# Kernel optimization log

Measured on AMD Instinct MI355X. Metric: run time of the kernel, lower is better.

Reference implementation:

```python
import jax, jax.numpy as jnp
import numpy as np

B, S, D = 8, 2048, 1024  # batch, seq_len, emb_dim == qkv_dim
NEG = -999999.0  # module uses -999999 instead of -inf


def setup_inputs() -> dict:
    key = jax.random.key(0)
    ks = jax.random.split(key, 4)
    inputs = jax.random.normal(ks[0], (B, S, D), dtype=jnp.float32)
    # causal mask, flax attention layout [B, 1, S, S]
    causal = jnp.tril(jnp.ones((S, S), dtype=bool))
    mask = jnp.broadcast_to(causal, (B, 1, S, S))
    scale = 1.0 / np.sqrt(D)
    Wq = jax.random.normal(ks[1], (D, D), dtype=jnp.float32) * scale
    Wk = jax.random.normal(ks[2], (D, D), dtype=jnp.float32) * scale
    Wv = jax.random.normal(ks[3], (D, D), dtype=jnp.float32) * scale
    z = jnp.zeros((D,), dtype=jnp.float32)
    return {"inputs": inputs, "mask": mask, "Wq": Wq, "bq": z, "Wk": Wk,
            "bk": z, "Wv": Wv, "bv": z}


def reference(inputs, mask, Wq, bq, Wk, bk, Wv, bv):
    q = inputs @ Wq + bq  # [B,S,D]
    k = inputs @ Wk + bk
    v = inputs @ Wv + bv
    depth = q.shape[-1]
    q = q / jnp.sqrt(jnp.asarray(depth, q.dtype))
    attn = jnp.einsum('bqd,bkd->bqk', q, k)  # [B,S,S]
    attn = jnp.where(jnp.squeeze(mask, axis=1), attn, NEG)
    attn = jax.nn.softmax(attn, axis=-1)
    return attn @ v  # [B,S,D]
```

## Files before the change

kernel.cpp:

```cpp
#include <hip/hip_runtime.h>
#include <hip/hip_bf16.h>
#include <cstdint>

#define S_LEN 2048
#define D_DIM 1024
#define NB 8

typedef __attribute__((ext_vector_type(8))) short bf16x8;
typedef __attribute__((ext_vector_type(4))) float f32x4;

__device__ __forceinline__ unsigned short f2bf(float f) {
  union { float f; unsigned u; } x; x.f = f;
  unsigned r = x.u + 0x7fffu + ((x.u >> 16) & 1u);
  return (unsigned short)(r >> 16);
}
__device__ __forceinline__ float bf2f(unsigned short b) {
  union { unsigned u; float f; } x; x.u = ((unsigned)b) << 16;
  return x.f;
}
__device__ __forceinline__ void gload16(const void* g, void* l) {
  __builtin_amdgcn_global_load_lds((const __attribute__((address_space(1))) void*)g,
                                   (__attribute__((address_space(3))) void*)l, 16, 0, 0);
}

__global__ __launch_bounds__(256)
void cvt_f32_bf16(const float* __restrict__ in, unsigned short* __restrict__ out, int n4) {
  int i = blockIdx.x * blockDim.x + threadIdx.x;
  if (i >= n4) return;
  float4 v = reinterpret_cast<const float4*>(in)[i];
  ushort4 o;
  o.x = f2bf(v.x); o.y = f2bf(v.y); o.z = f2bf(v.z); o.w = f2bf(v.w);
  reinterpret_cast<ushort4*>(out)[i] = o;
}

__global__ __launch_bounds__(256)
void transpose_f32_bf16(const float* __restrict__ in, unsigned short* __restrict__ out,
                        int rows, int cols) {
  __shared__ unsigned short tile[32][33];
  int bx = blockIdx.x * 32, by = blockIdx.y * 32;
  int tx = threadIdx.x, ty = threadIdx.y;
  #pragma unroll
  for (int i = ty; i < 32; i += 8)
    tile[i][tx] = f2bf(in[(size_t)(by + i) * cols + bx + tx]);
  __syncthreads();
  #pragma unroll
  for (int i = ty; i < 32; i += 8)
    out[(size_t)(bx + i) * rows + by + tx] = tile[tx][i];
}

__global__ __launch_bounds__(256)
void transpose_bf16(const unsigned short* __restrict__ in, unsigned short* __restrict__ out,
                    int ldin, int ldout, long zin, long zout) {
  __shared__ unsigned short tile[32][33];
  const unsigned short* ip = in + (size_t)blockIdx.z * zin;
  unsigned short* op = out + (size_t)blockIdx.z * zout;
  int bx = blockIdx.x * 32, by = blockIdx.y * 32;
  int tx = threadIdx.x, ty = threadIdx.y;
  #pragma unroll
  for (int i = ty; i < 32; i += 8)
    tile[i][tx] = ip[(size_t)(by + i) * ldin + bx + tx];
  __syncthreads();
  #pragma unroll
  for (int i = ty; i < 32; i += 8)
    op[(size_t)(bx + i) * ldout + by + tx] = tile[tx][i];
}

__global__ __launch_bounds__(256)
void combine_pv(float* __restrict__ O, const unsigned short* __restrict__ part,
                const float* __restrict__ rs) {
  int i = blockIdx.x * 256 + threadIdx.x;
  if (i >= 2097152) return;
  int e = i * 4;
  int z = e >> 20;
  int rem = e & 1048575;
  int r = rem >> 10;
  int col = rem & 1023;
  float inv = 1.f / rs[z * S_LEN + 1024 + r];
  float4 o = *reinterpret_cast<const float4*>(&O[(size_t)z * S_LEN * D_DIM + (size_t)(1024 + r) * 1024 + col]);
  ushort4 p = *reinterpret_cast<const ushort4*>(&part[((size_t)z * 1024 + r) * 1024 + col]);
  o.x = (o.x + bf2f(p.x)) * inv;
  o.y = (o.y + bf2f(p.y)) * inv;
  o.z = (o.z + bf2f(p.z)) * inv;
  o.w = (o.w + bf2f(p.w)) * inv;
  *reinterpret_cast<float4*>(&O[(size_t)z * S_LEN * D_DIM + (size_t)(1024 + r) * 1024 + col]) = o;
}

template<int MODE>
__global__ __launch_bounds__(512, 2)
void gemm8(const unsigned short* __restrict__ Aall, const unsigned short* __restrict__ Btall,
           void* __restrict__ Call, int Kd, int lda, int ldb, int ldc,
           long sAz, long sBz, long sCz,
           const float* __restrict__ b0, const float* __restrict__ b1,
           const float* __restrict__ b2, float* __restrict__ rowsum,
           unsigned short* __restrict__ part, int ntn) {
  __shared__ __align__(16) unsigned short As[4][8192];
  __shared__ __align__(16) unsigned short Bs[4][8192];
  int nwg = gridDim.x, bid = blockIdx.x;
  int wg = (bid & 7) * (nwg >> 3) + (bid >> 3);
  int z, tm, tn, kt0, nkt, m2c = 0;
  if (MODE == 0) {
    z = 0; tm = wg / ntn; tn = wg % ntn; kt0 = 0; nkt = Kd >> 5;
  } else if (MODE == 1) {
    z = wg / 36; int f = wg % 36;
    tm = 0;
    while ((tm + 1) * (tm + 2) / 2 <= f) ++tm;
    tn = f - tm * (tm + 1) / 2;
    kt0 = 0; nkt = Kd >> 5;
  } else {
    z = wg / 48; int r = wg % 48; tn = r / 12; int f = r % 12;
    const int tmT[12] = {0,1,2,3,4,4,5,5,6,6,7,7};
    const int cT[12]  = {0,0,0,0,0,1,0,1,0,1,0,1};
    tm = tmT[f]; int c = cT[f];
    int kts = (tm + 1) * 8;
    if (tm < 4) { kt0 = 0; nkt = kts; m2c = 0; }
    else { int half = kts >> 1; kt0 = c ? half : 0; nkt = c ? (kts - half) : half; m2c = 1 + c; }
  }
  const unsigned short* A  = Aall  + (size_t)z * sAz;
  const unsigned short* Bt = Btall + (size_t)z * sBz;
  int m0 = tm * 256, n0 = tn * 256;
  int t = threadIdx.x, lane = t & 63, w = t >> 6;
  int wr = w >> 2, wc = w & 3;
  int lr = lane & 15, lq = lane >> 4;
  long triBase = (long)(tm * (tm + 1) / 2) * 65536;

  int offA[8], offB[4];
  #pragma unroll
  for (int mi = 0; mi < 8; ++mi) {
    int row = wr * 128 + mi * 16 + lr;
    offA[mi] = row * 32 + ((lq ^ ((row >> 1) & 3)) * 8);
  }
  #pragma unroll
  for (int ni = 0; ni < 4; ++ni) {
    int row = wc * 64 + ni * 16 + lr;
    offB[ni] = row * 32 + ((lq ^ ((row >> 1) & 3)) * 8);
  }
  int srow[2], soff[2];
  #pragma unroll
  for (int c = 0; c < 2; ++c) {
    int r = c * 128 + w * 16 + (lane >> 2);
    srow[c] = r;
    soff[c] = ((lane & 3) ^ ((r >> 1) & 3)) * 8;
  }

  f32x4 acc[8][4];
  f32x4 zero4 = {0.f, 0.f, 0.f, 0.f};
  #pragma unroll
  for (int mi = 0; mi < 8; ++mi)
    #pragma unroll
    for (int ni = 0; ni < 4; ++ni) acc[mi][ni] = zero4;

  auto stgA = [&](int buf, int kg) {
    #pragma unroll
    for (int c = 0; c < 2; ++c) {
      const unsigned short* src;
      if (MODE == 2)
        src = A + triBase + (long)(kg >> 3) * 65536 + srow[c] * 256 + (kg & 7) * 32 + soff[c];
      else
        src = A + (size_t)(m0 + srow[c]) * lda + kg * 32 + soff[c];
      gload16(src, &As[buf][c * 4096 + w * 512]);
    }
  };
  auto stgB = [&](int buf, int kg) {
    #pragma unroll
    for (int c = 0; c < 2; ++c)
      gload16(Bt + (size_t)(n0 + srow[c]) * ldb + kg * 32 + soff[c],
              &Bs[buf][c * 4096 + w * 512]);
  };

  stgA(0, kt0); stgB(0, kt0); stgA(1, kt0 + 1); stgB(1, kt0 + 1);
  asm volatile("s_waitcnt vmcnt(4)" ::: "memory");
  __builtin_amdgcn_s_barrier();

  for (int i = 0; i < nkt; ++i) {
    const int bcur = i & 3, bpre = (i + 2) & 3;
    const bool stg = (i + 2 < nkt);
    const int kg = kt0 + i;
    const unsigned short* Ac = As[bcur];
    const unsigned short* Bc = Bs[bcur];
    bf16x8 af[4], bfv[4];

    #pragma unroll
    for (int q = 0; q < 4; ++q) af[q]  = *reinterpret_cast<const bf16x8*>(&Ac[offA[q]]);
    #pragma unroll
    for (int q = 0; q < 4; ++q) bfv[q] = *reinterpret_cast<const bf16x8*>(&Bc[offB[q]]);
    if (stg) stgA(bpre, kg + 2);
    __builtin_amdgcn_s_barrier();
    asm volatile("s_waitcnt lgkmcnt(0)" ::: "memory");
    __builtin_amdgcn_sched_barrier(0);
    __builtin_amdgcn_s_setprio(1);
    #pragma unroll
    for (int q = 0; q < 4; ++q)
      #pragma unroll
      for (int j = 0; j < 4; ++j)
        acc[q][j] = __builtin_amdgcn_mfma_f32_16x16x32_bf16(af[q], bfv[j], acc[q][j], 0, 0, 0);
    __builtin_amdgcn_s_setprio(0);
    __builtin_amdgcn_s_barrier();

    #pragma unroll
    for (int q = 0; q < 4; ++q) af[q] = *reinterpret_cast<const bf16x8*>(&Ac[offA[4 + q]]);
    if (stg) stgB(bpre, kg + 2);
    if (i + 2 < nkt)      asm volatile("s_waitcnt vmcnt(4)" ::: "memory");
    else if (i + 1 < nkt) asm volatile("s_waitcnt vmcnt(0)" ::: "memory");
    __builtin_amdgcn_s_barrier();
    asm volatile("s_waitcnt lgkmcnt(0)" ::: "memory");
    __builtin_amdgcn_sched_barrier(0);
    __builtin_amdgcn_s_setprio(1);
    #pragma unroll
    for (int q = 0; q < 4; ++q)
      #pragma unroll
      for (int j = 0; j < 4; ++j)
        acc[4 + q][j] = __builtin_amdgcn_mfma_f32_16x16x32_bf16(af[q], bfv[j], acc[4 + q][j], 0, 0, 0);
    __builtin_amdgcn_s_setprio(0);
    __builtin_amdgcn_s_barrier();
  }
  __syncthreads();

  unsigned short* ep = &As[0][0] + w * 4096;
  int lq4 = lq << 4;

  if (MODE == 0) {
    unsigned short* C = (unsigned short*)Call;
    #pragma unroll
    for (int mh = 0; mh < 2; ++mh) {
      #pragma unroll
      for (int mi2 = 0; mi2 < 4; ++mi2)
        #pragma unroll
        for (int ni = 0; ni < 4; ++ni) {
          int col = ni * 16 + lr;
          int gcol = n0 + wc * 64 + col;
          float bb, sc;
          if (gcol < 1024)      { bb = b0[gcol];        sc = 0.03125f; }
          else if (gcol < 2048) { bb = b1[gcol - 1024]; sc = 1.0f; }
          else                  { bb = b2[gcol - 2048]; sc = 1.0f; }
          #pragma unroll
          for (int j = 0; j < 4; ++j) {
            int lrow = mi2 * 16 + lq * 4 + j;
            ep[lrow * 64 + (col ^ lq4)] = f2bf((acc[mh * 4 + mi2][ni][j] + bb) * sc);
          }
        }
      asm volatile("s_waitcnt lgkmcnt(0)" ::: "memory");
      #pragma unroll
      for (int pass = 0; pass < 8; ++pass) {
        int rrow = pass * 8 + (lane >> 3);
        int c8 = (lane & 7) * 8;
        int sw = ((rrow >> 2) & 3) << 4;
        bf16x8 vv = *reinterpret_cast<const bf16x8*>(&ep[rrow * 64 + (c8 ^ sw)]);
        int grow = m0 + wr * 128 + mh * 64 + rrow;
        *reinterpret_cast<bf16x8*>(&C[(size_t)grow * ldc + n0 + wc * 64 + c8]) = vv;
      }
      asm volatile("s_waitcnt lgkmcnt(0)" ::: "memory");
    }
  } else if (MODE == 1) {
    unsigned short* Ct = (unsigned short*)Call + (size_t)z * sCz + triBase + (long)tn * 65536;
    float* rs = rowsum + z * S_LEN;
    #pragma unroll
    for (int mh = 0; mh < 2; ++mh) {
      #pragma unroll
      for (int mi2 = 0; mi2 < 4; ++mi2)
        #pragma unroll
        for (int j = 0; j < 4; ++j) {
          int lrow = mi2 * 16 + lq * 4 + j;
          int grow = m0 + wr * 128 + mh * 64 + lrow;
          float partial = 0.f;
          #pragma unroll
          for (int ni = 0; ni < 4; ++ni) {
            int col = ni * 16 + lr;
            int gcol = n0 + wc * 64 + col;
            float e = (gcol <= grow) ? __expf(acc[mh * 4 + mi2][ni][j]) : 0.f;
            partial += e;
            ep[lrow * 64 + (col ^ lq4)] = f2bf(e);
          }
          #pragma unroll
          for (int off = 1; off < 16; off <<= 1) partial += __shfl_xor(partial, off);
          if (lr == 0) atomicAdd(&rs[grow], partial);
        }
      asm volatile("s_waitcnt lgkmcnt(0)" ::: "memory");
      #pragma unroll
      for (int pass = 0; pass < 8; ++pass) {
        int rrow = pass * 8 + (lane >> 3);
        int c8 = (lane & 7) * 8;
        int sw = ((rrow >> 2) & 3) << 4;
        bf16x8 vv = *reinterpret_cast<const bf16x8*>(&ep[rrow * 64 + (c8 ^ sw)]);
        int lrow2 = wr * 128 + mh * 64 + rrow;
        *reinterpret_cast<bf16x8*>(&Ct[(size_t)lrow2 * 256 + wc * 64 + c8]) = vv;
      }
      asm volatile("s_waitcnt lgkmcnt(0)" ::: "memory");
    }
  } else {
    float* C = (float*)Call + (size_t)z * sCz;
    const float* rs = rowsum + z * S_LEN;
    #pragma unroll
    for (int mi = 0; mi < 8; ++mi)
      #pragma unroll
      for (int j = 0; j < 4; ++j) {
        int row = m0 + wr * 128 + mi * 16 + lq * 4 + j;
        if (m2c == 0) {
          float inv = 1.f / rs[row];
          #pragma unroll
          for (int ni = 0; ni < 4; ++ni) {
            int col = n0 + wc * 64 + ni * 16 + lr;
            C[(size_t)row * ldc + col] = acc[mi][ni][j] * inv;
          }
        } else if (m2c == 1) {
          #pragma unroll
          for (int ni = 0; ni < 4; ++ni) {
            int col = n0 + wc * 64 + ni * 16 + lr;
            C[(size_t)row * ldc + col] = acc[mi][ni][j];
          }
        } else {
          unsigned short* P = part + ((size_t)z * 1024 + (row - 1024)) * 1024;
          #pragma unroll
          for (int ni = 0; ni < 4; ++ni) {
            int col = n0 + wc * 64 + ni * 16 + lr;
            P[col] = f2bf(acc[mi][ni][j]);
          }
        }
      }
  }
}

extern "C" void kernel_launch(void* const* d_in, const int* in_sizes, int n_in,
                              void* d_out, int out_size, void* d_ws, size_t ws_size,
                              hipStream_t stream) {
  (void)in_sizes; (void)n_in; (void)out_size; (void)ws_size;
  const float* X  = (const float*)d_in[0];
  const float* Wq = (const float*)d_in[2];
  const float* bq = (const float*)d_in[3];
  const float* Wk = (const float*)d_in[4];
  const float* bk = (const float*)d_in[5];
  const float* Wv = (const float*)d_in[6];
  const float* bv = (const float*)d_in[7];

  char* ws = (char*)d_ws;
  unsigned short* Xb  = (unsigned short*)(ws);
  unsigned short* Wt  = (unsigned short*)(ws + 33554432L);
  float*          Rs  = (float*)(ws + 33554432L);
  unsigned short* QKV = (unsigned short*)(ws + 39845888L);
  unsigned short* Pb  = (unsigned short*)(ws + 140509184L);
  unsigned short* Prt = (unsigned short*)(ws + 178257920L);
  unsigned short* Vt  = Xb;

  cvt_f32_bf16<<<16384, 256, 0, stream>>>(X, Xb, (NB * S_LEN * D_DIM) / 4);
  dim3 tb(32, 8);
  transpose_f32_bf16<<<dim3(32, 32), tb, 0, stream>>>(Wq, Wt + 0L * 1048576L, D_DIM, D_DIM);
  transpose_f32_bf16<<<dim3(32, 32), tb, 0, stream>>>(Wk, Wt + 1L * 1048576L, D_DIM, D_DIM);
  transpose_f32_bf16<<<dim3(32, 32), tb, 0, stream>>>(Wv, Wt + 2L * 1048576L, D_DIM, D_DIM);
  gemm8<0><<<dim3(64 * 12, 1, 1), 512, 0, stream>>>(Xb, Wt, (void*)QKV,
      D_DIM, D_DIM, D_DIM, 3 * D_DIM,
      0L, 0L, 0L, bq, bk, bv, nullptr, nullptr, 12);
  hipMemsetAsync(Rs, 0, NB * S_LEN * sizeof(float), stream);
  gemm8<1><<<dim3(288, 1, 1), 512, 0, stream>>>(QKV, QKV + 1024, (void*)Pb,
      D_DIM, 3 * D_DIM, 3 * D_DIM, 256,
      (long)S_LEN * 3 * D_DIM, (long)S_LEN * 3 * D_DIM, 36L * 65536L,
      nullptr, nullptr, nullptr, Rs, nullptr, 0);
  transpose_bf16<<<dim3(32, 64, NB), tb, 0, stream>>>(QKV + 2048, Vt,
      3 * D_DIM, S_LEN, (long)S_LEN * 3 * D_DIM, (long)D_DIM * S_LEN);
  gemm8<2><<<dim3(384, 1, 1), 512, 0, stream>>>(Pb, Vt, d_out,
      S_LEN, 0, S_LEN, D_DIM,
      36L * 65536L, (long)D_DIM * S_LEN, (long)S_LEN * D_DIM,
      nullptr, nullptr, nullptr, Rs, Prt, 0);
  combine_pv<<<8192, 256, 0, stream>>>((float*)d_out, Prt, Rs);
}
```

Before: 329.2 us.

## Split score GEMM into 256x128 causal tiles with dedicated kernel and pointer-increment staging

Replaces the MODE 1 score GEMM (256x256 lower-triangular tiles, 288 blocks) with a dedicated gemm_sc kernel that uses 256x128 tiles over the causal region, giving 576 blocks and finer triangular coverage. The P buffer layout and the PV GEMM's A addressing change to match the new 32768-element tile blocks. Global-load addresses are now advanced by pointer increments instead of being recomputed each stage. The three weight transposes are merged into one launch. Narrower tiles give more parallelism and skip some above-diagonal work, at the cost of lower arithmetic intensity per tile.

```diff
diff --git a/kernel.cpp b/kernel.cpp
--- a/kernel.cpp
+++ b/kernel.cpp
@@ -34,18 +34,20 @@
 }
 
 __global__ __launch_bounds__(256)
-void transpose_f32_bf16(const float* __restrict__ in, unsigned short* __restrict__ out,
-                        int rows, int cols) {
+void transpose_w3(const float* __restrict__ W0, const float* __restrict__ W1,
+                  const float* __restrict__ W2, unsigned short* __restrict__ out) {
   __shared__ unsigned short tile[32][33];
+  const float* in = (blockIdx.z == 0) ? W0 : (blockIdx.z == 1 ? W1 : W2);
+  unsigned short* o = out + (size_t)blockIdx.z * 1048576;
   int bx = blockIdx.x * 32, by = blockIdx.y * 32;
   int tx = threadIdx.x, ty = threadIdx.y;
   #pragma unroll
   for (int i = ty; i < 32; i += 8)
-    tile[i][tx] = f2bf(in[(size_t)(by + i) * cols + bx + tx]);
+    tile[i][tx] = f2bf(in[(size_t)(by + i) * D_DIM + bx + tx]);
   __syncthreads();
   #pragma unroll
   for (int i = ty; i < 32; i += 8)
-    out[(size_t)(bx + i) * rows + by + tx] = tile[tx][i];
+    o[(size_t)(bx + i) * D_DIM + by + tx] = tile[tx][i];
 }
 
 __global__ __launch_bounds__(256)
@@ -91,7 +93,7 @@
            void* __restrict__ Call, int Kd, int lda, int ldb, int ldc,
            long sAz, long sBz, long sCz,
            const float* __restrict__ b0, const float* __restrict__ b1,
-           const float* __restrict__ b2, float* __restrict__ rowsum,
+           const float* __restrict__ b2, const float* __restrict__ rowsum,
            unsigned short* __restrict__ part, int ntn) {
   __shared__ __align__(16) unsigned short As[4][8192];
   __shared__ __align__(16) unsigned short Bs[4][8192];
@@ -100,12 +102,6 @@
   int z, tm, tn, kt0, nkt, m2c = 0;
   if (MODE == 0) {
     z = 0; tm = wg / ntn; tn = wg % ntn; kt0 = 0; nkt = Kd >> 5;
-  } else if (MODE == 1) {
-    z = wg / 36; int f = wg % 36;
-    tm = 0;
-    while ((tm + 1) * (tm + 2) / 2 <= f) ++tm;
-    tn = f - tm * (tm + 1) / 2;
-    kt0 = 0; nkt = Kd >> 5;
   } else {
     z = wg / 48; int r = wg % 48; tn = r / 12; int f = r % 12;
     const int tmT[12] = {0,1,2,3,4,4,5,5,6,6,7,7};
@@ -121,7 +117,6 @@
   int t = threadIdx.x, lane = t & 63, w = t >> 6;
   int wr = w >> 2, wc = w & 3;
   int lr = lane & 15, lq = lane >> 4;
-  long triBase = (long)(tm * (tm + 1) / 2) * 65536;
 
   int offA[8], offB[4];
   #pragma unroll
@@ -142,6 +137,18 @@
     soff[c] = ((lane & 3) ^ ((r >> 1) & 3)) * 8;
   }
 
+  const char *pA0, *pA1, *pB0, *pB1;
+  if (MODE == 2) {
+    size_t tb = (size_t)tm * (tm + 1) * 65536 + (size_t)(kt0 >> 2) * 65536;
+    pA0 = (const char*)A + tb + srow[0] * 256 + ((kt0 & 3) * 32 + soff[0]) * 2;
+    pA1 = (const char*)A + tb + srow[1] * 256 + ((kt0 & 3) * 32 + soff[1]) * 2;
+  } else {
+    pA0 = (const char*)(A + (size_t)(m0 + srow[0]) * lda + kt0 * 32 + soff[0]);
+    pA1 = (const char*)(A + (size_t)(m0 + srow[1]) * lda + kt0 * 32 + soff[1]);
+  }
+  pB0 = (const char*)(Bt + (size_t)(n0 + srow[0]) * ldb + kt0 * 32 + soff[0]);
+  pB1 = (const char*)(Bt + (size_t)(n0 + srow[1]) * ldb + kt0 * 32 + soff[1]);
+
   f32x4 acc[8][4];
   f32x4 zero4 = {0.f, 0.f, 0.f, 0.f};
   #pragma unroll
@@ -149,32 +156,28 @@
     #pragma unroll
     for (int ni = 0; ni < 4; ++ni) acc[mi][ni] = zero4;
 
-  auto stgA = [&](int buf, int kg) {
-    #pragma unroll
-    for (int c = 0; c < 2; ++c) {
-      const unsigned short* src;
-      if (MODE == 2)
-        src = A + triBase + (long)(kg >> 3) * 65536 + srow[c] * 256 + (kg & 7) * 32 + soff[c];
-      else
-        src = A + (size_t)(m0 + srow[c]) * lda + kg * 32 + soff[c];
-      gload16(src, &As[buf][c * 4096 + w * 512]);
-    }
+  auto stgA = [&](int buf) {
+    gload16(pA0, &As[buf][w * 512]);
+    gload16(pA1, &As[buf][4096 + w * 512]);
   };
-  auto stgB = [&](int buf, int kg) {
-    #pragma unroll
-    for (int c = 0; c < 2; ++c)
-      gload16(Bt + (size_t)(n0 + srow[c]) * ldb + kg * 32 + soff[c],
-              &Bs[buf][c * 4096 + w * 512]);
+  auto stgB = [&](int buf) {
+    gload16(pB0, &Bs[buf][w * 512]);
+    gload16(pB1, &Bs[buf][4096 + w * 512]);
   };
-
-  stgA(0, kt0); stgB(0, kt0); stgA(1, kt0 + 1); stgB(1, kt0 + 1);
+  auto advA = [&](int s) {
+    long d = (MODE == 2) ? (((s & 3) == 3) ? 65344L : 64L) : 64L;
+    pA0 += d; pA1 += d;
+  };
+  auto advB = [&]() { pB0 += 64; pB1 += 64; };
+
+  stgA(0); advA(kt0); stgB(0); advB();
+  stgA(1); advA(kt0 + 1); stgB(1); advB();
   asm volatile("s_waitcnt vmcnt(4)" ::: "memory");
   __builtin_amdgcn_s_barrier();
 
   for (int i = 0; i < nkt; ++i) {
     const int bcur = i & 3, bpre = (i + 2) & 3;
     const bool stg = (i + 2 < nkt);
-    const int kg = kt0 + i;
     const unsigned short* Ac = As[bcur];
     const unsigned short* Bc = Bs[bcur];
     bf16x8 af[4], bfv[4];
@@ -183,7 +186,7 @@
     for (int q = 0; q < 4; ++q) af[q]  = *reinterpret_cast<const bf16x8*>(&Ac[offA[q]]);
     #pragma unroll
     for (int q = 0; q < 4; ++q) bfv[q] = *reinterpret_cast<const bf16x8*>(&Bc[offB[q]]);
-    if (stg) stgA(bpre, kg + 2);
+    if (stg) { stgA(bpre); advA(kt0 + i + 2); }
     __builtin_amdgcn_s_barrier();
     asm volatile("s_waitcnt lgkmcnt(0)" ::: "memory");
     __builtin_amdgcn_sched_barrier(0);
@@ -198,7 +201,7 @@
 
     #pragma unroll
     for (int q = 0; q < 4; ++q) af[q] = *reinterpret_cast<const bf16x8*>(&Ac[offA[4 + q]]);
-    if (stg) stgB(bpre, kg + 2);
+    if (stg) { stgB(bpre); advB(); }
     if (i + 2 < nkt)      asm volatile("s_waitcnt vmcnt(4)" ::: "memory");
     else if (i + 1 < nkt) asm volatile("s_waitcnt vmcnt(0)" ::: "memory");
     __builtin_amdgcn_s_barrier();
@@ -247,42 +250,6 @@
         bf16x8 vv = *reinterpret_cast<const bf16x8*>(&ep[rrow * 64 + (c8 ^ sw)]);
         int grow = m0 + wr * 128 + mh * 64 + rrow;
         *reinterpret_cast<bf16x8*>(&C[(size_t)grow * ldc + n0 + wc * 64 + c8]) = vv;
-      }
-      asm volatile("s_waitcnt lgkmcnt(0)" ::: "memory");
-    }
-  } else if (MODE == 1) {
-    unsigned short* Ct = (unsigned short*)Call + (size_t)z * sCz + triBase + (long)tn * 65536;
-    float* rs = rowsum + z * S_LEN;
-    #pragma unroll
-    for (int mh = 0; mh < 2; ++mh) {
-      #pragma unroll
-      for (int mi2 = 0; mi2 < 4; ++mi2)
-        #pragma unroll
-        for (int j = 0; j < 4; ++j) {
-          int lrow = mi2 * 16 + lq * 4 + j;
-          int grow = m0 + wr * 128 + mh * 64 + lrow;
-          float partial = 0.f;
-          #pragma unroll
-          for (int ni = 0; ni < 4; ++ni) {
-            int col = ni * 16 + lr;
-            int gcol = n0 + wc * 64 + col;
-            float e = (gcol <= grow) ? __expf(acc[mh * 4 + mi2][ni][j]) : 0.f;
-            partial += e;
-            ep[lrow * 64 + (col ^ lq4)] = f2bf(e);
-          }
-          #pragma unroll
-          for (int off = 1; off < 16; off <<= 1) partial += __shfl_xor(partial, off);
-          if (lr == 0) atomicAdd(&rs[grow], partial);
-        }
-      asm volatile("s_waitcnt lgkmcnt(0)" ::: "memory");
-      #pragma unroll
-      for (int pass = 0; pass < 8; ++pass) {
-        int rrow = pass * 8 + (lane >> 3);
-        int c8 = (lane & 7) * 8;
-        int sw = ((rrow >> 2) & 3) << 4;
-        bf16x8 vv = *reinterpret_cast<const bf16x8*>(&ep[rrow * 64 + (c8 ^ sw)]);
-        int lrow2 = wr * 128 + mh * 64 + rrow;
-        *reinterpret_cast<bf16x8*>(&Ct[(size_t)lrow2 * 256 + wc * 64 + c8]) = vv;
       }
       asm volatile("s_waitcnt lgkmcnt(0)" ::: "memory");
     }
@@ -319,6 +286,151 @@
   }
 }
 
+__global__ __launch_bounds__(512, 2)
+void gemm_sc(const unsigned short* __restrict__ QKV, unsigned short* __restrict__ Pb,
+             float* __restrict__ rowsum) {
+  __shared__ __align__(16) unsigned short As[4][8192];
+  __shared__ __align__(16) unsigned short Bs4[4][4096];
+  int bid = blockIdx.x;
+  int wg = (bid & 7) * 72 + (bid >> 3);
+  int z = wg / 72, f = wg % 72;
+  int tm = 0;
+  while ((tm + 1) * (tm + 2) <= f) ++tm;
+  int ct = f - tm * (tm + 1);
+  const unsigned short* A  = QKV + (size_t)z * S_LEN * 3072;
+  const unsigned short* Bt = QKV + 1024 + (size_t)z * S_LEN * 3072;
+  int m0 = tm * 256, n0 = ct * 128;
+  int t = threadIdx.x, lane = t & 63, w = t >> 6;
+  int wr = w >> 2, wc = w & 3;
+  int lr = lane & 15, lq = lane >> 4;
+  const int nkt = 32;
+
+  int offA[8], offB[2];
+  #pragma unroll
+  for (int mi = 0; mi < 8; ++mi) {
+    int row = wr * 128 + mi * 16 + lr;
+    offA[mi] = row * 32 + ((lq ^ ((row >> 1) & 3)) * 8);
+  }
+  #pragma unroll
+  for (int ni = 0; ni < 2; ++ni) {
+    int row = wc * 32 + ni * 16 + lr;
+    offB[ni] = row * 32 + ((lq ^ ((row >> 1) & 3)) * 8);
+  }
+  int srow[2], soff[2];
+  #pragma unroll
+  for (int c = 0; c < 2; ++c) {
+    int r = c * 128 + w * 16 + (lane >> 2);
+    srow[c] = r;
+    soff[c] = ((lane & 3) ^ ((r >> 1) & 3)) * 8;
+  }
+  int rB = w * 16 + (lane >> 2);
+  int soffB = ((lane & 3) ^ ((rB >> 1) & 3)) * 8;
+
+  const char* pA0 = (const char*)(A + (size_t)(m0 + srow[0]) * 3072 + soff[0]);
+  const char* pA1 = (const char*)(A + (size_t)(m0 + srow[1]) * 3072 + soff[1]);
+  const char* pB  = (const char*)(Bt + (size_t)(n0 + rB) * 3072 + soffB);
+
+  f32x4 acc[8][2];
+  f32x4 zero4 = {0.f, 0.f, 0.f, 0.f};
+  #pragma unroll
+  for (int mi = 0; mi < 8; ++mi) { acc[mi][0] = zero4; acc[mi][1] = zero4; }
+
+  auto stgA = [&](int buf) {
+    gload16(pA0, &As[buf][w * 512]);
+    gload16(pA1, &As[buf][4096 + w * 512]);
+    pA0 += 64; pA1 += 64;
+  };
+  auto stgB = [&](int buf) {
+    gload16(pB, &Bs4[buf][w * 512]);
+    pB += 64;
+  };
+
+  stgA(0); stgB(0); stgA(1); stgB(1);
+  asm volatile("s_waitcnt vmcnt(3)" ::: "memory");
+  __builtin_amdgcn_s_barrier();
+
+  for (int i = 0; i < nkt; ++i) {
+    const int bcur = i & 3, bpre = (i + 2) & 3;
+    const bool stg = (i + 2 < nkt);
+    const unsigned short* Ac = As[bcur];
+    const unsigned short* Bc = Bs4[bcur];
+    bf16x8 af[4], bfv[2];
+
+    #pragma unroll
+    for (int q = 0; q < 4; ++q) af[q] = *reinterpret_cast<const bf16x8*>(&Ac[offA[q]]);
+    bfv[0] = *reinterpret_cast<const bf16x8*>(&Bc[offB[0]]);
+    bfv[1] = *reinterpret_cast<const bf16x8*>(&Bc[offB[1]]);
+    if (stg) stgA(bpre);
+    __builtin_amdgcn_s_barrier();
+    asm volatile("s_waitcnt lgkmcnt(0)" ::: "memory");
+    __builtin_amdgcn_sched_barrier(0);
+    __builtin_amdgcn_s_setprio(1);
+    #pragma unroll
+    for (int q = 0; q < 4; ++q) {
+      acc[q][0] = __builtin_amdgcn_mfma_f32_16x16x32_bf16(af[q], bfv[0], acc[q][0], 0, 0, 0);
+      acc[q][1] = __builtin_amdgcn_mfma_f32_16x16x32_bf16(af[q], bfv[1], acc[q][1], 0, 0, 0);
+    }
+    __builtin_amdgcn_s_setprio(0);
+    __builtin_amdgcn_s_barrier();
+
+    #pragma unroll
+    for (int q = 0; q < 4; ++q) af[q] = *reinterpret_cast<const bf16x8*>(&Ac[offA[4 + q]]);
+    if (stg) stgB(bpre);
+    if (i + 2 < nkt)      asm volatile("s_waitcnt vmcnt(3)" ::: "memory");
+    else if (i + 1 < nkt) asm volatile("s_waitcnt vmcnt(0)" ::: "memory");
+    __builtin_amdgcn_s_barrier();
+    asm volatile("s_waitcnt lgkmcnt(0)" ::: "memory");
+    __builtin_amdgcn_sched_barrier(0);
+    __builtin_amdgcn_s_setprio(1);
+    #pragma unroll
+    for (int q = 0; q < 4; ++q) {
+      acc[4 + q][0] = __builtin_amdgcn_mfma_f32_16x16x32_bf16(af[q], bfv[0], acc[4 + q][0], 0, 0, 0);
+      acc[4 + q][1] = __builtin_amdgcn_mfma_f32_16x16x32_bf16(af[q], bfv[1], acc[4 + q][1], 0, 0, 0);
+    }
+    __builtin_amdgcn_s_setprio(0);
+    __builtin_amdgcn_s_barrier();
+  }
+  __syncthreads();
+
+  unsigned short* ep = &As[0][0] + w * 2304;
+  unsigned short* Ct = Pb + (size_t)z * (72L * 32768) + (size_t)(tm * (tm + 1) + ct) * 32768;
+  float* rs = rowsum + z * S_LEN;
+  #pragma unroll
+  for (int mh = 0; mh < 2; ++mh) {
+    #pragma unroll
+    for (int mi2 = 0; mi2 < 4; ++mi2)
+      #pragma unroll
+      for (int j = 0; j < 4; ++j) {
+        int lrow = mi2 * 16 + lq * 4 + j;
+        int grow = m0 + wr * 128 + mh * 64 + lrow;
+        float partial = 0.f;
+        #pragma unroll
+        for (int ni = 0; ni < 2; ++ni) {
+          int col = ni * 16 + lr;
+          int gcol = n0 + wc * 32 + col;
+          float e = (gcol <= grow) ? __expf(acc[mh * 4 + mi2][ni][j]) : 0.f;
+          partial += e;
+          ep[lrow * 36 + col] = f2bf(e);
+        }
+        #pragma unroll
+        for (int off = 1; off < 16; off <<= 1) partial += __shfl_xor(partial, off);
+        if (lr == 0) atomicAdd(&rs[grow], partial);
+      }
+    asm volatile("s_waitcnt lgkmcnt(0)" ::: "memory");
+    __builtin_amdgcn_sched_barrier(0);
+    #pragma unroll
+    for (int pass = 0; pass < 4; ++pass) {
+      int rrow = pass * 16 + (lane >> 2);
+      int c8 = (lane & 3) * 8;
+      bf16x8 vv = *reinterpret_cast<const bf16x8*>(&ep[rrow * 36 + c8]);
+      int lrow2 = wr * 128 + mh * 64 + rrow;
+      *reinterpret_cast<bf16x8*>(&Ct[(size_t)lrow2 * 128 + wc * 32 + c8]) = vv;
+    }
+    asm volatile("s_waitcnt lgkmcnt(0)" ::: "memory");
+    __builtin_amdgcn_sched_barrier(0);
+  }
+}
+
 extern "C" void kernel_launch(void* const* d_in, const int* in_sizes, int n_in,
                               void* d_out, int out_size, void* d_ws, size_t ws_size,
                               hipStream_t stream) {
@@ -342,22 +454,17 @@
 
   cvt_f32_bf16<<<16384, 256, 0, stream>>>(X, Xb, (NB * S_LEN * D_DIM) / 4);
   dim3 tb(32, 8);
-  transpose_f32_bf16<<<dim3(32, 32), tb, 0, stream>>>(Wq, Wt + 0L * 1048576L, D_DIM, D_DIM);
-  transpose_f32_bf16<<<dim3(32, 32), tb, 0, stream>>>(Wk, Wt + 1L * 1048576L, D_DIM, D_DIM);
-  transpose_f32_bf16<<<dim3(32, 32), tb, 0, stream>>>(Wv, Wt + 2L * 1048576L, D_DIM, D_DIM);
+  transpose_w3<<<dim3(32, 32, 3), tb, 0, stream>>>(Wq, Wk, Wv, Wt);
   gemm8<0><<<dim3(64 * 12, 1, 1), 512, 0, stream>>>(Xb, Wt, (void*)QKV,
       D_DIM, D_DIM, D_DIM, 3 * D_DIM,
       0L, 0L, 0L, bq, bk, bv, nullptr, nullptr, 12);
   hipMemsetAsync(Rs, 0, NB * S_LEN * sizeof(float), stream);
-  gemm8<1><<<dim3(288, 1, 1), 512, 0, stream>>>(QKV, QKV + 1024, (void*)Pb,
-      D_DIM, 3 * D_DIM, 3 * D_DIM, 256,
-      (long)S_LEN * 3 * D_DIM, (long)S_LEN * 3 * D_DIM, 36L * 65536L,
-      nullptr, nullptr, nullptr, Rs, nullptr, 0);
+  gemm_sc<<<dim3(576, 1, 1), 512, 0, stream>>>(QKV, Pb, Rs);
   transpose_bf16<<<dim3(32, 64, NB), tb, 0, stream>>>(QKV + 2048, Vt,
       3 * D_DIM, S_LEN, (long)S_LEN * 3 * D_DIM, (long)D_DIM * S_LEN);
   gemm8<2><<<dim3(384, 1, 1), 512, 0, stream>>>(Pb, Vt, d_out,
       S_LEN, 0, S_LEN, D_DIM,
-      36L * 65536L, (long)D_DIM * S_LEN, (long)S_LEN * D_DIM,
+      72L * 32768L, (long)D_DIM * S_LEN, (long)S_LEN * D_DIM,
       nullptr, nullptr, nullptr, Rs, Prt, 0);
   combine_pv<<<8192, 256, 0, stream>>>((float*)d_out, Prt, Rs);
 }
```

Result: slower. 352.2 us (+7.0%).

## Merge prep kernels and fold V transpose into QK^T GEMM launch

Applied to the files above, without the earlier changes.

Combines the X conversion and three weight transposes into one prep kernel, cutting three launches. The V transpose also moves into extra workgroups appended to the QK^T GEMM grid, so it runs alongside the GEMM tiles instead of as a separate launch. This saves launch gaps and idle tail time. In exchange, the transpose blocks use the GEMM's 512-thread, heavy-LDS configuration, which may lower their efficiency or compete with the GEMM tiles for CUs.

```diff
diff --git a/kernel.cpp b/kernel.cpp
--- a/kernel.cpp
+++ b/kernel.cpp
@@ -24,45 +24,31 @@
 }
 
 __global__ __launch_bounds__(256)
-void cvt_f32_bf16(const float* __restrict__ in, unsigned short* __restrict__ out, int n4) {
-  int i = blockIdx.x * blockDim.x + threadIdx.x;
-  if (i >= n4) return;
-  float4 v = reinterpret_cast<const float4*>(in)[i];
-  ushort4 o;
-  o.x = f2bf(v.x); o.y = f2bf(v.y); o.z = f2bf(v.z); o.w = f2bf(v.w);
-  reinterpret_cast<ushort4*>(out)[i] = o;
-}
-
-__global__ __launch_bounds__(256)
-void transpose_f32_bf16(const float* __restrict__ in, unsigned short* __restrict__ out,
-                        int rows, int cols) {
+void prep(const float* __restrict__ X, const float* __restrict__ W0,
+          const float* __restrict__ W1, const float* __restrict__ W2,
+          unsigned short* __restrict__ Xb, unsigned short* __restrict__ Wt) {
   __shared__ unsigned short tile[32][33];
-  int bx = blockIdx.x * 32, by = blockIdx.y * 32;
-  int tx = threadIdx.x, ty = threadIdx.y;
+  int bid = blockIdx.x, tid = threadIdx.x;
+  if (bid < 16384) {
+    int i = bid * 256 + tid;
+    float4 v = reinterpret_cast<const float4*>(X)[i];
+    ushort4 o;
+    o.x = f2bf(v.x); o.y = f2bf(v.y); o.z = f2bf(v.z); o.w = f2bf(v.w);
+    reinterpret_cast<ushort4*>(Xb)[i] = o;
+    return;
+  }
+  int f = bid - 16384;
+  int zc = f >> 10, rem = f & 1023, by = (rem >> 5) * 32, bx = (rem & 31) * 32;
+  const float* in = (zc == 0) ? W0 : (zc == 1 ? W1 : W2);
+  unsigned short* o = Wt + (size_t)zc * 1048576;
+  int tx = tid & 31, ty = tid >> 5;
   #pragma unroll
   for (int i = ty; i < 32; i += 8)
-    tile[i][tx] = f2bf(in[(size_t)(by + i) * cols + bx + tx]);
+    tile[i][tx] = f2bf(in[(size_t)(by + i) * D_DIM + bx + tx]);
   __syncthreads();
   #pragma unroll
   for (int i = ty; i < 32; i += 8)
-    out[(size_t)(bx + i) * rows + by + tx] = tile[tx][i];
-}
-
-__global__ __launch_bounds__(256)
-void transpose_bf16(const unsigned short* __restrict__ in, unsigned short* __restrict__ out,
-                    int ldin, int ldout, long zin, long zout) {
-  __shared__ unsigned short tile[32][33];
-  const unsigned short* ip = in + (size_t)blockIdx.z * zin;
-  unsigned short* op = out + (size_t)blockIdx.z * zout;
-  int bx = blockIdx.x * 32, by = blockIdx.y * 32;
-  int tx = threadIdx.x, ty = threadIdx.y;
-  #pragma unroll
-  for (int i = ty; i < 32; i += 8)
-    tile[i][tx] = ip[(size_t)(by + i) * ldin + bx + tx];
-  __syncthreads();
-  #pragma unroll
-  for (int i = ty; i < 32; i += 8)
-    op[(size_t)(bx + i) * ldout + by + tx] = tile[tx][i];
+    o[(size_t)(bx + i) * D_DIM + by + tx] = tile[tx][i];
 }
 
 __global__ __launch_bounds__(256)
@@ -95,7 +81,31 @@
            unsigned short* __restrict__ part, int ntn) {
   __shared__ __align__(16) unsigned short As[4][8192];
   __shared__ __align__(16) unsigned short Bs[4][8192];
-  int nwg = gridDim.x, bid = blockIdx.x;
+  int bid = blockIdx.x;
+  int t = threadIdx.x, lane = t & 63, w = t >> 6;
+
+  if (MODE == 1 && bid >= 288) {
+    int v = bid - 288;
+    int z = v >> 5, c0 = (v & 31) * 32;
+    const unsigned short* V = Aall + (size_t)z * sAz + 2048;
+    unsigned short* out = part + (size_t)z * (1024L * 2048) + (size_t)c0 * 2048;
+    unsigned short* tl = &As[0][0];
+    int tx = t & 31, ty = t >> 5;
+    int i2 = t & 63, j0 = t >> 6;
+    for (int r0 = 0; r0 < S_LEN; r0 += 64) {
+      #pragma unroll
+      for (int ii = ty; ii < 64; ii += 16)
+        tl[ii * 33 + tx] = V[(size_t)(r0 + ii) * 3072 + c0 + tx];
+      __syncthreads();
+      #pragma unroll
+      for (int jj = j0; jj < 32; jj += 8)
+        out[(size_t)jj * 2048 + r0 + i2] = tl[i2 * 33 + jj];
+      __syncthreads();
+    }
+    return;
+  }
+
+  int nwg = (MODE == 1) ? 288 : gridDim.x;
   int wg = (bid & 7) * (nwg >> 3) + (bid >> 3);
   int z, tm, tn, kt0, nkt, m2c = 0;
   if (MODE == 0) {
@@ -118,7 +128,6 @@
   const unsigned short* A  = Aall  + (size_t)z * sAz;
   const unsigned short* Bt = Btall + (size_t)z * sBz;
   int m0 = tm * 256, n0 = tn * 256;
-  int t = threadIdx.x, lane = t & 63, w = t >> 6;
   int wr = w >> 2, wc = w & 3;
   int lr = lane & 15, lq = lane >> 4;
   long triBase = (long)(tm * (tm + 1) / 2) * 65536;
@@ -340,21 +349,15 @@
   unsigned short* Prt = (unsigned short*)(ws + 178257920L);
   unsigned short* Vt  = Xb;
 
-  cvt_f32_bf16<<<16384, 256, 0, stream>>>(X, Xb, (NB * S_LEN * D_DIM) / 4);
-  dim3 tb(32, 8);
-  transpose_f32_bf16<<<dim3(32, 32), tb, 0, stream>>>(Wq, Wt + 0L * 1048576L, D_DIM, D_DIM);
-  transpose_f32_bf16<<<dim3(32, 32), tb, 0, stream>>>(Wk, Wt + 1L * 1048576L, D_DIM, D_DIM);
-  transpose_f32_bf16<<<dim3(32, 32), tb, 0, stream>>>(Wv, Wt + 2L * 1048576L, D_DIM, D_DIM);
+  prep<<<19456, 256, 0, stream>>>(X, Wq, Wk, Wv, Xb, Wt);
   gemm8<0><<<dim3(64 * 12, 1, 1), 512, 0, stream>>>(Xb, Wt, (void*)QKV,
       D_DIM, D_DIM, D_DIM, 3 * D_DIM,
       0L, 0L, 0L, bq, bk, bv, nullptr, nullptr, 12);
   hipMemsetAsync(Rs, 0, NB * S_LEN * sizeof(float), stream);
-  gemm8<1><<<dim3(288, 1, 1), 512, 0, stream>>>(QKV, QKV + 1024, (void*)Pb,
+  gemm8<1><<<dim3(288 + 256, 1, 1), 512, 0, stream>>>(QKV, QKV + 1024, (void*)Pb,
       D_DIM, 3 * D_DIM, 3 * D_DIM, 256,
       (long)S_LEN * 3 * D_DIM, (long)S_LEN * 3 * D_DIM, 36L * 65536L,
-      nullptr, nullptr, nullptr, Rs, nullptr, 0);
-  transpose_bf16<<<dim3(32, 64, NB), tb, 0, stream>>>(QKV + 2048, Vt,
-      3 * D_DIM, S_LEN, (long)S_LEN * 3 * D_DIM, (long)D_DIM * S_LEN);
+      nullptr, nullptr, nullptr, Rs, Vt, 0);
   gemm8<2><<<dim3(384, 1, 1), 512, 0, stream>>>(Pb, Vt, d_out,
       S_LEN, 0, S_LEN, D_DIM,
       36L * 65536L, (long)D_DIM * S_LEN, (long)S_LEN * D_DIM,
```

Result: faster. 319.4 us (-3.0%).
